# Kernel optimization log

Measured on AMD Instinct MI355X. Metric: run time of the kernel, lower is better.

The kernel has to match this reference:

```python
import jax, jax.numpy as jnp
import numpy as np
from jax import lax

SIGMA = 5
RADIUS = int(4 * SIGMA + 0.5)  # 20 -> kernel size 41, pad_size = 41//2 = 20 = RADIUS
D_AP = 2.27
D_DV = 2.27


def _gauss_d1_kernel():
    # gaussian_kernel1d(sigma, order=1, radius): q(x) = -x/sigma^2, kernel = q(x)*phi(x)
    x = np.arange(-RADIUS, RADIUS + 1).astype(np.float64)
    phi = np.exp(-0.5 / SIGMA ** 2 * x ** 2)
    phi = phi / phi.sum()
    return ((-x / SIGMA ** 2) * phi).astype(np.float32)

_KERNEL = jnp.asarray(_gauss_d1_kernel())


def _conv1d_valid(x, k):
    # x: [N, L], k: [K] -> [N, L-K+1]; cross-correlation, same as torch F.conv1d
    return lax.conv_general_dilated(x[:, None, :], k[None, None, :], (1,), 'VALID')[:, 0, :]


def diffY(x):
    # circular padding along H, derivative / dDV
    c, h, w = x.shape
    xp = jnp.pad(x, ((0, 0), (RADIUS, RADIUS), (0, 0)), mode='wrap')
    xp = jnp.transpose(xp, (0, 2, 1)).reshape(c * w, h + 2 * RADIUS)
    out = _conv1d_valid(xp, _KERNEL).reshape(c, w, h)
    return jnp.transpose(out, (0, 2, 1)) / D_DV


def diffX(x):
    # reflect padding along W, derivative / dAP
    c, h, w = x.shape
    xp = jnp.pad(x, ((0, 0), (0, 0), (RADIUS, RADIUS)), mode='reflect')
    out = _conv1d_valid(xp.reshape(c * h, w + 2 * RADIUS), _KERNEL).reshape(c, h, w)
    return out / D_AP


def setup_inputs() -> dict:
    key = jax.random.key(0)
    k1, k2, k3, k4, k5 = jax.random.split(key, 5)
    H, W = 1024, 2048
    return {
        'y': jax.random.normal(k1, (5, H, W), dtype=jnp.float32),
        'v': jax.random.normal(k2, (2, H, W), dtype=jnp.float32),
        'gamma_ds': jax.random.normal(k3, (H, W), dtype=jnp.float32),
        'cad_coefs': jax.random.uniform(k4, (3,), dtype=jnp.float32),
        'myo_coefs': jax.random.uniform(k5, (5,), dtype=jnp.float32),
    }


def reference(y, v, gamma_ds, cad_coefs, myo_coefs):
    H, W = y.shape[-2:]
    m4 = y[:4]                                  # [4,H,W] myosin components
    c1 = y[4:]                                  # [1,H,W] cadherin

    d1_m = jnp.stack([diffY(m4), diffX(m4)], axis=-1).reshape(2, 2, H, W, 2)
    m = m4.reshape(2, 2, H, W)
    d1_c = jnp.stack([diffY(c1), diffX(c1)], axis=-1).reshape(H, W, 2)
    c = c1[0]

    d1_v = jnp.stack([diffY(v), diffX(v)], axis=-1)   # [2,H,W,2]: d1_v[i,y,x,j] = d_j v_i
    gv = jnp.einsum('iyxj->ijyx', d1_v)
    gvT = jnp.einsum('jyxi->ijyx', d1_v)
    O = -0.5 * (gv - gvT)                       # vorticity
    E = 0.5 * (gv + gvT)                        # strain rate

    eye = jnp.eye(2, dtype=y.dtype)[:, :, None, None]
    trm_yx = jnp.einsum('kkyx->yx', m)
    deviatoric = m - 0.5 * trm_yx[None, None] * eye

    m_norm = jnp.sqrt(jnp.sum(m * m, axis=(0, 1), keepdims=True))            # [1,1,H,W]
    m_0 = jnp.mean(m_norm, axis=(2, 3), keepdims=True)                       # [1,1,1,1]
    dev_mag = jnp.sqrt(jnp.sum(deviatoric * deviatoric, axis=(0, 1), keepdims=True))
    devE = jnp.einsum('klyx,klyx->yx', deviatoric, E)[None, None]

    E_active = E - jnp.sign(devE) * devE * deviatoric / dev_mag ** 2
    E_active = 0.5 * E_active * dev_mag / m_0
    E_passive = E - E_active

    mE = (jnp.einsum('ikyx,kjyx->ijyx', m, E_passive)
          + jnp.einsum('ikyx,kjyx->ijyx', E_passive, m))

    cad = jax.nn.relu(cad_coefs)
    myo = jax.nn.relu(myo_coefs)

    cdot = (-jnp.einsum('iyx,yxi->yx', v, d1_c)
            - cad[0] * c
            + cad[1] * c * jnp.einsum('iyxi->yx', d1_v)
            + cad[2] * gamma_ds)

    trm = trm_yx[None, None]
    gamma_dv = jnp.array([[1.0, 0.0], [0.0, 0.0]], dtype=y.dtype)[:, :, None, None]

    mdot = (-jnp.einsum('kyx,ijyxk->ijyx', v, d1_m)
            - jnp.einsum('ikyx,kjyx->ijyx', O, m)
            + jnp.einsum('ikyx,kjyx->ijyx', m, O)
            - myo[0] * m
            + myo[1] * mE
            - myo[2] * c[None, None] * mE
            + myo[3] * trm * gamma_dv
            + myo[4] * trm * m)

    return jnp.concatenate([mdot.reshape(4, H, W), cdot[None]], axis=0)
```

## Files before the change

### kernel.cpp

```cpp
#include <hip/hip_runtime.h>
#include <math.h>

#define RAD 20
#define KLEN 41
#define NH 1024
#define NW 2048
#define NHW (NH * NW)

struct KW { float w[KLEN]; };
constexpr double cexp_neg(double u) {
  double term = 1.0, sum = 1.0;
  for (int k = 1; k < 30; ++k) { term *= (-u) / (double)k; sum += term; }
  return sum;
}
constexpr KW make_kw() {
  KW r{};
  double ph[KLEN] = {};
  double s = 0.0;
  for (int i = 0; i < KLEN; ++i) {
    double d = (double)(i - RAD);
    double e = cexp_neg(d * d / 800.0);
    e = e * e; e = e * e; e = e * e; e = e * e;
    ph[i] = e; s += e;
  }
  for (int i = 0; i < KLEN; ++i) {
    double d = (double)(i - RAD);
    r.w[i] = (float)((-d / 25.0) * (ph[i] / s) / 2.27);
  }
  return r;
}
static constexpr KW KWC = make_kw();

template <int K>
__device__ __forceinline__ void tap(float s, float& r0, float& r1, float& r2,
                                    float& r3, float& r4, float& r5, float& r6,
                                    float& r7) {
  if constexpr (K - 0 >= 0 && K - 0 <= 40) r0 = fmaf(s, KWC.w[K - 0], r0);
  if constexpr (K - 1 >= 0 && K - 1 <= 40) r1 = fmaf(s, KWC.w[K - 1], r1);
  if constexpr (K - 2 >= 0 && K - 2 <= 40) r2 = fmaf(s, KWC.w[K - 2], r2);
  if constexpr (K - 3 >= 0 && K - 3 <= 40) r3 = fmaf(s, KWC.w[K - 3], r3);
  if constexpr (K - 4 >= 0 && K - 4 <= 40) r4 = fmaf(s, KWC.w[K - 4], r4);
  if constexpr (K - 5 >= 0 && K - 5 <= 40) r5 = fmaf(s, KWC.w[K - 5], r5);
  if constexpr (K - 6 >= 0 && K - 6 <= 40) r6 = fmaf(s, KWC.w[K - 6], r6);
  if constexpr (K - 7 >= 0 && K - 7 <= 40) r7 = fmaf(s, KWC.w[K - 7], r7);
}

#define R8 r0, r1, r2, r3, r4, r5, r6, r7

__global__ __launch_bounds__(256) void k_reduce(const float* __restrict__ y,
                                                double* __restrict__ acc) {
  const int tid = blockIdx.x * blockDim.x + threadIdx.x;
  const int stride = gridDim.x * blockDim.x;
  double local = 0.0;
  for (int i = tid; i < NHW; i += stride) {
    float a = y[i];
    float b = y[i + NHW];
    float c = y[i + 2 * (size_t)NHW];
    float d = y[i + 3 * (size_t)NHW];
    local += (double)sqrtf(a * a + b * b + c * c + d * d);
  }
#pragma unroll
  for (int off = 32; off > 0; off >>= 1) local += __shfl_down(local, off, 64);
  __shared__ double smem[4];
  const int lane = threadIdx.x & 63;
  const int wid = threadIdx.x >> 6;
  if (lane == 0) smem[wid] = local;
  __syncthreads();
  if (threadIdx.x == 0) {
    double s = smem[0] + smem[1] + smem[2] + smem[3];
    atomicAdd(acc, s);
  }
}

__global__ __launch_bounds__(256) void k_dx(const float* __restrict__ y,
                                            const float* __restrict__ v,
                                            float* __restrict__ ws) {
  __shared__ float row[2120];
  const int t = threadIdx.x;
  const int r = blockIdx.x;
  const int ch = blockIdx.y;
  const float* src = (ch < 5) ? (y + (size_t)ch * NHW) : (v + (size_t)(ch - 5) * NHW);
  const float* rp = src + (size_t)r * NW;

#define SWZ(i) ((i) + ((i) >> 6))
#define ST(i, val) { const int ii_ = (i); row[SWZ(ii_)] = (val); }

  const float4* rp4 = (const float4*)rp;
  float4 b0 = rp4[t];
  float4 b1 = rp4[t + 256];
  ST(RAD + 4 * t + 0, b0.x)
  ST(RAD + 4 * t + 1, b0.y)
  ST(RAD + 4 * t + 2, b0.z)
  ST(RAD + 4 * t + 3, b0.w)
  ST(RAD + 4 * (t + 256) + 0, b1.x)
  ST(RAD + 4 * (t + 256) + 1, b1.y)
  ST(RAD + 4 * (t + 256) + 2, b1.z)
  ST(RAD + 4 * (t + 256) + 3, b1.w)
  if (t < RAD) {
    ST(t, rp[RAD - t])
    ST(NW + RAD + t, rp[NW - 2 - t])
  }
  __syncthreads();

  const int xb = 8 * t;
  float r0 = 0.f, r1 = 0.f, r2 = 0.f, r3 = 0.f;
  float r4 = 0.f, r5 = 0.f, r6 = 0.f, r7 = 0.f;
#define RD(k) { const int x_ = xb + (k); float s_ = row[SWZ(x_)]; tap<(k)>(s_, R8); }
  RD(0)  RD(1)  RD(2)  RD(3)  RD(4)  RD(5)  RD(6)  RD(7)
  RD(8)  RD(9)  RD(10) RD(11) RD(12) RD(13) RD(14) RD(15)
  RD(16) RD(17) RD(18) RD(19) RD(20) RD(21) RD(22) RD(23)
  RD(24) RD(25) RD(26) RD(27) RD(28) RD(29) RD(30) RD(31)
  RD(32) RD(33) RD(34) RD(35) RD(36) RD(37) RD(38) RD(39)
  RD(40) RD(41) RD(42) RD(43) RD(44) RD(45) RD(46) RD(47)
#undef RD

  float4 o0, o1;
  o0.x = r0; o0.y = r1; o0.z = r2; o0.w = r3;
  o1.x = r4; o1.y = r5; o1.z = r6; o1.w = r7;
  float4* dst = (float4*)(ws + (size_t)(7 + ch) * NHW + (size_t)r * NW + xb);
  dst[0] = o0;
  dst[1] = o1;
}

#define TW 64
#define TH 32

__global__ __launch_bounds__(256) void k_dy(const float* __restrict__ y,
                                            const float* __restrict__ v,
                                            float* __restrict__ ws) {
  __shared__ float tile[(TH + 2 * RAD) * TW];
  const int lane = threadIdx.x & 63;
  const int wid = threadIdx.x >> 6;
  const int x0 = blockIdx.x * TW;
  const int yb = blockIdx.y * TH;
  const int ch = blockIdx.z;
  const float* src = (ch < 5) ? (y + (size_t)ch * NHW) : (v + (size_t)(ch - 5) * NHW);

#define GLD(k) src[(size_t)(((yb - RAD + wid + 4 * (k)) + NH) & (NH - 1)) * NW + x0 + lane]
  float t0 = GLD(0), t1 = GLD(1), t2 = GLD(2), t3 = GLD(3), t4 = GLD(4);
  float t5 = GLD(5), t6 = GLD(6), t7 = GLD(7), t8 = GLD(8), t9 = GLD(9);
  float t10 = GLD(10), t11 = GLD(11), t12 = GLD(12), t13 = GLD(13);
  float t14 = GLD(14), t15 = GLD(15), t16 = GLD(16), t17 = GLD(17);
#define TST(k, val) tile[(wid + 4 * (k)) * TW + lane] = val;
  TST(0, t0)  TST(1, t1)  TST(2, t2)  TST(3, t3)  TST(4, t4)  TST(5, t5)
  TST(6, t6)  TST(7, t7)  TST(8, t8)  TST(9, t9)  TST(10, t10) TST(11, t11)
  TST(12, t12) TST(13, t13) TST(14, t14) TST(15, t15) TST(16, t16) TST(17, t17)
  __syncthreads();

  const int base = wid * 8;
  float r0 = 0.f, r1 = 0.f, r2 = 0.f, r3 = 0.f;
  float r4 = 0.f, r5 = 0.f, r6 = 0.f, r7 = 0.f;
#define DYCHUNK(c)                                                   \
  {                                                                  \
    float s0 = tile[(base + 4 * (c) + 0) * TW + lane];               \
    float s1 = tile[(base + 4 * (c) + 1) * TW + lane];               \
    float s2 = tile[(base + 4 * (c) + 2) * TW + lane];               \
    float s3 = tile[(base + 4 * (c) + 3) * TW + lane];               \
    tap<4 * (c) + 0>(s0, R8);                                        \
    tap<4 * (c) + 1>(s1, R8);                                        \
    tap<4 * (c) + 2>(s2, R8);                                        \
    tap<4 * (c) + 3>(s3, R8);                                        \
  }
  DYCHUNK(0) DYCHUNK(1) DYCHUNK(2) DYCHUNK(3) DYCHUNK(4) DYCHUNK(5)
  DYCHUNK(6) DYCHUNK(7) DYCHUNK(8) DYCHUNK(9) DYCHUNK(10) DYCHUNK(11)

  float* dst = ws + (size_t)ch * NHW + (size_t)(yb + base) * NW + x0 + lane;
  dst[0] = r0;
  dst[(size_t)NW] = r1;
  dst[2 * (size_t)NW] = r2;
  dst[3 * (size_t)NW] = r3;
  dst[4 * (size_t)NW] = r4;
  dst[5 * (size_t)NW] = r5;
  dst[6 * (size_t)NW] = r6;
  dst[7 * (size_t)NW] = r7;
}

__global__ __launch_bounds__(256) void k_final(
    const float* __restrict__ y, const float* __restrict__ v,
    const float* __restrict__ gds, const float* __restrict__ cadc,
    const float* __restrict__ myoc, const float* __restrict__ ws,
    const double* __restrict__ acc, float* __restrict__ out) {
  const size_t i = (size_t)blockIdx.x * blockDim.x + threadIdx.x;
  if (i >= NHW) return;

  const float m0 = (float)(acc[0] / (double)NHW);
  const float cad0 = fmaxf(cadc[0], 0.f);
  const float cad1 = fmaxf(cadc[1], 0.f);
  const float cad2 = fmaxf(cadc[2], 0.f);
  const float my0 = fmaxf(myoc[0], 0.f);
  const float my1 = fmaxf(myoc[1], 0.f);
  const float my2 = fmaxf(myoc[2], 0.f);
  const float my3 = fmaxf(myoc[3], 0.f);
  const float my4 = fmaxf(myoc[4], 0.f);

  const float m00 = y[i];
  const float m01 = y[i + (size_t)NHW];
  const float m10 = y[i + 2 * (size_t)NHW];
  const float m11 = y[i + 3 * (size_t)NHW];
  const float c = y[i + 4 * (size_t)NHW];
  const float v0 = v[i];
  const float v1 = v[i + (size_t)NHW];
  const float g = gds[i];

  const float dY_m00 = ws[i];
  const float dY_m01 = ws[i + (size_t)NHW];
  const float dY_m10 = ws[i + 2 * (size_t)NHW];
  const float dY_m11 = ws[i + 3 * (size_t)NHW];
  const float dY_c = ws[i + 4 * (size_t)NHW];
  const float dY_v0 = ws[i + 5 * (size_t)NHW];
  const float dY_v1 = ws[i + 6 * (size_t)NHW];
  const float dX_m00 = ws[i + 7 * (size_t)NHW];
  const float dX_m01 = ws[i + 8 * (size_t)NHW];
  const float dX_m10 = ws[i + 9 * (size_t)NHW];
  const float dX_m11 = ws[i + 10 * (size_t)NHW];
  const float dX_c = ws[i + 11 * (size_t)NHW];
  const float dX_v0 = ws[i + 12 * (size_t)NHW];
  const float dX_v1 = ws[i + 13 * (size_t)NHW];

  const float gv00 = dY_v0, gv01 = dX_v0, gv10 = dY_v1, gv11 = dX_v1;
  const float ww = -0.5f * (gv01 - gv10);
  const float E00 = gv00, E11 = gv11;
  const float E01 = 0.5f * (gv01 + gv10);
  const float E10 = E01;

  const float trm = m00 + m11;
  const float dev00 = m00 - 0.5f * trm;
  const float dev01 = m01;
  const float dev10 = m10;
  const float dev11 = m11 - 0.5f * trm;
  const float dmag_sq = dev00 * dev00 + dev01 * dev01 + dev10 * dev10 + dev11 * dev11;
  const float dm = sqrtf(dmag_sq);
  const float dm2 = dm * dm;
  const float devE = dev00 * E00 + dev01 * E01 + dev10 * E10 + dev11 * E11;
  const float sg = (devE > 0.f) ? 1.f : ((devE < 0.f) ? -1.f : 0.f);
  const float coef = sg * devE / dm2;
  const float sc = 0.5f * dm / m0;

  const float Ea00 = (E00 - coef * dev00) * sc;
  const float Ea01 = (E01 - coef * dev01) * sc;
  const float Ea10 = (E10 - coef * dev10) * sc;
  const float Ea11 = (E11 - coef * dev11) * sc;
  const float Ep00 = E00 - Ea00;
  const float Ep01 = E01 - Ea01;
  const float Ep10 = E10 - Ea10;
  const float Ep11 = E11 - Ea11;

  const float mE00 = (m00 * Ep00 + m01 * Ep10) + (Ep00 * m00 + Ep01 * m10);
  const float mE01 = (m00 * Ep01 + m01 * Ep11) + (Ep00 * m01 + Ep01 * m11);
  const float mE10 = (m10 * Ep00 + m11 * Ep10) + (Ep10 * m00 + Ep11 * m10);
  const float mE11 = (m10 * Ep01 + m11 * Ep11) + (Ep10 * m01 + Ep11 * m11);

  const float divv = gv00 + gv11;
  const float cdot = -(v0 * dY_c + v1 * dX_c) - cad0 * c + cad1 * c * divv + cad2 * g;

  const float md00 = -(v0 * dY_m00 + v1 * dX_m00) - ww * m10 - ww * m01 - my0 * m00 +
                     my1 * mE00 - my2 * c * mE00 + my3 * trm + my4 * trm * m00;
  const float md01 = -(v0 * dY_m01 + v1 * dX_m01) - ww * m11 + ww * m00 - my0 * m01 +
                     my1 * mE01 - my2 * c * mE01 + my4 * trm * m01;
  const float md10 = -(v0 * dY_m10 + v1 * dX_m10) + ww * m00 - ww * m11 - my0 * m10 +
                     my1 * mE10 - my2 * c * mE10 + my4 * trm * m10;
  const float md11 = -(v0 * dY_m11 + v1 * dX_m11) + ww * m01 + ww * m10 - my0 * m11 +
                     my1 * mE11 - my2 * c * mE11 + my4 * trm * m11;

  out[i] = md00;
  out[i + (size_t)NHW] = md01;
  out[i + 2 * (size_t)NHW] = md10;
  out[i + 3 * (size_t)NHW] = md11;
  out[i + 4 * (size_t)NHW] = cdot;
}

extern "C" void kernel_launch(void* const* d_in, const int* in_sizes, int n_in,
                              void* d_out, int out_size, void* d_ws, size_t ws_size,
                              hipStream_t stream) {
  (void)in_sizes; (void)n_in; (void)out_size; (void)ws_size;
  const float* y = (const float*)d_in[0];
  const float* v = (const float*)d_in[1];
  const float* gds = (const float*)d_in[2];
  const float* cadc = (const float*)d_in[3];
  const float* myoc = (const float*)d_in[4];
  float* out = (float*)d_out;

  double* acc = (double*)d_ws;
  float* planes = (float*)((char*)d_ws + 512);

  hipMemsetAsync(acc, 0, sizeof(double), stream);
  k_reduce<<<dim3(1024), dim3(256), 0, stream>>>(y, acc);
  k_dx<<<dim3(NH, 7), dim3(256), 0, stream>>>(y, v, planes);
  k_dy<<<dim3(NW / TW, NH / TH, 7), dim3(256), 0, stream>>>(y, v, planes);
  k_final<<<dim3(NHW / 256), dim3(256), 0, stream>>>(y, v, gds, cadc, myoc, planes, acc, out);
}
```

Before: 202.1 us.

## Fuse Y-derivative convolution into final pointwise kernel and vectorize reduction loads

Merges the vertical Gaussian-derivative stencil kernel with the final pointwise kernel. Y-derivatives for all seven channels now stay in registers instead of being written to and read back from seven workspace planes, and c, v0 and v1 are read from the shared tile. The shared tile grows to four channels (about 73 KB) and each thread holds 56 accumulators, which may reduce occupancy. The reduction kernel also switches to float4 loads.

```diff
diff --git a/kernel.cpp b/kernel.cpp
--- a/kernel.cpp
+++ b/kernel.cpp
@@ -47,17 +47,44 @@
 
 #define R8 r0, r1, r2, r3, r4, r5, r6, r7
 
+#define TW 64
+#define TH 32
+#define TILE_CH ((TH + 2 * RAD) * TW)
+
+__device__ __forceinline__ void conv_col(const float* __restrict__ t, int base,
+                                         int lane, float& r0, float& r1,
+                                         float& r2, float& r3, float& r4,
+                                         float& r5, float& r6, float& r7) {
+#define CCHUNK(c)                                      \
+  {                                                    \
+    float s0 = t[(base + 4 * (c) + 0) * TW + lane];    \
+    float s1 = t[(base + 4 * (c) + 1) * TW + lane];    \
+    float s2 = t[(base + 4 * (c) + 2) * TW + lane];    \
+    float s3 = t[(base + 4 * (c) + 3) * TW + lane];    \
+    tap<4 * (c) + 0>(s0, R8);                          \
+    tap<4 * (c) + 1>(s1, R8);                          \
+    tap<4 * (c) + 2>(s2, R8);                          \
+    tap<4 * (c) + 3>(s3, R8);                          \
+  }
+  CCHUNK(0) CCHUNK(1) CCHUNK(2) CCHUNK(3) CCHUNK(4) CCHUNK(5)
+  CCHUNK(6) CCHUNK(7) CCHUNK(8) CCHUNK(9) CCHUNK(10) CCHUNK(11)
+#undef CCHUNK
+}
+
 __global__ __launch_bounds__(256) void k_reduce(const float* __restrict__ y,
                                                 double* __restrict__ acc) {
   const int tid = blockIdx.x * blockDim.x + threadIdx.x;
   const int stride = gridDim.x * blockDim.x;
   double local = 0.0;
-  for (int i = tid; i < NHW; i += stride) {
-    float a = y[i];
-    float b = y[i + NHW];
-    float c = y[i + 2 * (size_t)NHW];
-    float d = y[i + 3 * (size_t)NHW];
-    local += (double)sqrtf(a * a + b * b + c * c + d * d);
+  for (int q = tid; q < NHW / 4; q += stride) {
+    float4 a = ((const float4*)y)[q];
+    float4 b = ((const float4*)(y + NHW))[q];
+    float4 c = ((const float4*)(y + 2 * (size_t)NHW))[q];
+    float4 d = ((const float4*)(y + 3 * (size_t)NHW))[q];
+    local += (double)sqrtf(a.x * a.x + b.x * b.x + c.x * c.x + d.x * d.x);
+    local += (double)sqrtf(a.y * a.y + b.y * b.y + c.y * c.y + d.y * d.y);
+    local += (double)sqrtf(a.z * a.z + b.z * b.z + c.z * c.z + d.z * d.z);
+    local += (double)sqrtf(a.w * a.w + b.w * b.w + c.w * c.w + d.w * d.w);
   }
 #pragma unroll
   for (int off = 32; off > 0; off >>= 1) local += __shfl_down(local, off, 64);
@@ -122,66 +149,17 @@
   dst[1] = o1;
 }
 
-#define TW 64
-#define TH 32
-
-__global__ __launch_bounds__(256) void k_dy(const float* __restrict__ y,
-                                            const float* __restrict__ v,
-                                            float* __restrict__ ws) {
-  __shared__ float tile[(TH + 2 * RAD) * TW];
+__global__ __launch_bounds__(256) void k_dyf(
+    const float* __restrict__ y, const float* __restrict__ v,
+    const float* __restrict__ gds, const float* __restrict__ cadc,
+    const float* __restrict__ myoc, const float* __restrict__ ws,
+    const double* __restrict__ acc, float* __restrict__ out) {
+  __shared__ float tile[4 * TILE_CH];
   const int lane = threadIdx.x & 63;
   const int wid = threadIdx.x >> 6;
   const int x0 = blockIdx.x * TW;
   const int yb = blockIdx.y * TH;
-  const int ch = blockIdx.z;
-  const float* src = (ch < 5) ? (y + (size_t)ch * NHW) : (v + (size_t)(ch - 5) * NHW);
-
-#define GLD(k) src[(size_t)(((yb - RAD + wid + 4 * (k)) + NH) & (NH - 1)) * NW + x0 + lane]
-  float t0 = GLD(0), t1 = GLD(1), t2 = GLD(2), t3 = GLD(3), t4 = GLD(4);
-  float t5 = GLD(5), t6 = GLD(6), t7 = GLD(7), t8 = GLD(8), t9 = GLD(9);
-  float t10 = GLD(10), t11 = GLD(11), t12 = GLD(12), t13 = GLD(13);
-  float t14 = GLD(14), t15 = GLD(15), t16 = GLD(16), t17 = GLD(17);
-#define TST(k, val) tile[(wid + 4 * (k)) * TW + lane] = val;
-  TST(0, t0)  TST(1, t1)  TST(2, t2)  TST(3, t3)  TST(4, t4)  TST(5, t5)
-  TST(6, t6)  TST(7, t7)  TST(8, t8)  TST(9, t9)  TST(10, t10) TST(11, t11)
-  TST(12, t12) TST(13, t13) TST(14, t14) TST(15, t15) TST(16, t16) TST(17, t17)
-  __syncthreads();
-
   const int base = wid * 8;
-  float r0 = 0.f, r1 = 0.f, r2 = 0.f, r3 = 0.f;
-  float r4 = 0.f, r5 = 0.f, r6 = 0.f, r7 = 0.f;
-#define DYCHUNK(c)                                                   \
-  {                                                                  \
-    float s0 = tile[(base + 4 * (c) + 0) * TW + lane];               \
-    float s1 = tile[(base + 4 * (c) + 1) * TW + lane];               \
-    float s2 = tile[(base + 4 * (c) + 2) * TW + lane];               \
-    float s3 = tile[(base + 4 * (c) + 3) * TW + lane];               \
-    tap<4 * (c) + 0>(s0, R8);                                        \
-    tap<4 * (c) + 1>(s1, R8);                                        \
-    tap<4 * (c) + 2>(s2, R8);                                        \
-    tap<4 * (c) + 3>(s3, R8);                                        \
-  }
-  DYCHUNK(0) DYCHUNK(1) DYCHUNK(2) DYCHUNK(3) DYCHUNK(4) DYCHUNK(5)
-  DYCHUNK(6) DYCHUNK(7) DYCHUNK(8) DYCHUNK(9) DYCHUNK(10) DYCHUNK(11)
-
-  float* dst = ws + (size_t)ch * NHW + (size_t)(yb + base) * NW + x0 + lane;
-  dst[0] = r0;
-  dst[(size_t)NW] = r1;
-  dst[2 * (size_t)NW] = r2;
-  dst[3 * (size_t)NW] = r3;
-  dst[4 * (size_t)NW] = r4;
-  dst[5 * (size_t)NW] = r5;
-  dst[6 * (size_t)NW] = r6;
-  dst[7 * (size_t)NW] = r7;
-}
-
-__global__ __launch_bounds__(256) void k_final(
-    const float* __restrict__ y, const float* __restrict__ v,
-    const float* __restrict__ gds, const float* __restrict__ cadc,
-    const float* __restrict__ myoc, const float* __restrict__ ws,
-    const double* __restrict__ acc, float* __restrict__ out) {
-  const size_t i = (size_t)blockIdx.x * blockDim.x + threadIdx.x;
-  if (i >= NHW) return;
 
   const float m0 = (float)(acc[0] / (double)NHW);
   const float cad0 = fmaxf(cadc[0], 0.f);
@@ -193,80 +171,134 @@
   const float my3 = fmaxf(myoc[3], 0.f);
   const float my4 = fmaxf(myoc[4], 0.f);
 
-  const float m00 = y[i];
-  const float m01 = y[i + (size_t)NHW];
-  const float m10 = y[i + 2 * (size_t)NHW];
-  const float m11 = y[i + 3 * (size_t)NHW];
-  const float c = y[i + 4 * (size_t)NHW];
-  const float v0 = v[i];
-  const float v1 = v[i + (size_t)NHW];
-  const float g = gds[i];
-
-  const float dY_m00 = ws[i];
-  const float dY_m01 = ws[i + (size_t)NHW];
-  const float dY_m10 = ws[i + 2 * (size_t)NHW];
-  const float dY_m11 = ws[i + 3 * (size_t)NHW];
-  const float dY_c = ws[i + 4 * (size_t)NHW];
-  const float dY_v0 = ws[i + 5 * (size_t)NHW];
-  const float dY_v1 = ws[i + 6 * (size_t)NHW];
-  const float dX_m00 = ws[i + 7 * (size_t)NHW];
-  const float dX_m01 = ws[i + 8 * (size_t)NHW];
-  const float dX_m10 = ws[i + 9 * (size_t)NHW];
-  const float dX_m11 = ws[i + 10 * (size_t)NHW];
-  const float dX_c = ws[i + 11 * (size_t)NHW];
-  const float dX_v0 = ws[i + 12 * (size_t)NHW];
-  const float dX_v1 = ws[i + 13 * (size_t)NHW];
-
-  const float gv00 = dY_v0, gv01 = dX_v0, gv10 = dY_v1, gv11 = dX_v1;
-  const float ww = -0.5f * (gv01 - gv10);
-  const float E00 = gv00, E11 = gv11;
-  const float E01 = 0.5f * (gv01 + gv10);
-  const float E10 = E01;
-
-  const float trm = m00 + m11;
-  const float dev00 = m00 - 0.5f * trm;
-  const float dev01 = m01;
-  const float dev10 = m10;
-  const float dev11 = m11 - 0.5f * trm;
-  const float dmag_sq = dev00 * dev00 + dev01 * dev01 + dev10 * dev10 + dev11 * dev11;
-  const float dm = sqrtf(dmag_sq);
-  const float dm2 = dm * dm;
-  const float devE = dev00 * E00 + dev01 * E01 + dev10 * E10 + dev11 * E11;
-  const float sg = (devE > 0.f) ? 1.f : ((devE < 0.f) ? -1.f : 0.f);
-  const float coef = sg * devE / dm2;
-  const float sc = 0.5f * dm / m0;
-
-  const float Ea00 = (E00 - coef * dev00) * sc;
-  const float Ea01 = (E01 - coef * dev01) * sc;
-  const float Ea10 = (E10 - coef * dev10) * sc;
-  const float Ea11 = (E11 - coef * dev11) * sc;
-  const float Ep00 = E00 - Ea00;
-  const float Ep01 = E01 - Ea01;
-  const float Ep10 = E10 - Ea10;
-  const float Ep11 = E11 - Ea11;
-
-  const float mE00 = (m00 * Ep00 + m01 * Ep10) + (Ep00 * m00 + Ep01 * m10);
-  const float mE01 = (m00 * Ep01 + m01 * Ep11) + (Ep00 * m01 + Ep01 * m11);
-  const float mE10 = (m10 * Ep00 + m11 * Ep10) + (Ep10 * m00 + Ep11 * m10);
-  const float mE11 = (m10 * Ep01 + m11 * Ep11) + (Ep10 * m01 + Ep11 * m11);
-
-  const float divv = gv00 + gv11;
-  const float cdot = -(v0 * dY_c + v1 * dX_c) - cad0 * c + cad1 * c * divv + cad2 * g;
-
-  const float md00 = -(v0 * dY_m00 + v1 * dX_m00) - ww * m10 - ww * m01 - my0 * m00 +
-                     my1 * mE00 - my2 * c * mE00 + my3 * trm + my4 * trm * m00;
-  const float md01 = -(v0 * dY_m01 + v1 * dX_m01) - ww * m11 + ww * m00 - my0 * m01 +
-                     my1 * mE01 - my2 * c * mE01 + my4 * trm * m01;
-  const float md10 = -(v0 * dY_m10 + v1 * dX_m10) + ww * m00 - ww * m11 - my0 * m10 +
-                     my1 * mE10 - my2 * c * mE10 + my4 * trm * m10;
-  const float md11 = -(v0 * dY_m11 + v1 * dX_m11) + ww * m01 + ww * m10 - my0 * m11 +
-                     my1 * mE11 - my2 * c * mE11 + my4 * trm * m11;
-
-  out[i] = md00;
-  out[i + (size_t)NHW] = md01;
-  out[i + 2 * (size_t)NHW] = md10;
-  out[i + 3 * (size_t)NHW] = md11;
-  out[i + 4 * (size_t)NHW] = cdot;
+#define SGLD(sp, k) \
+  (sp)[(size_t)(((yb - RAD + wid + 4 * (k)) + NH) & (NH - 1)) * NW + x0 + lane]
+#define STAGECH(g, srcp)                                                    \
+  {                                                                         \
+    const float* sp_ = (srcp);                                              \
+    float u0 = SGLD(sp_, 0), u1 = SGLD(sp_, 1), u2 = SGLD(sp_, 2);          \
+    float u3 = SGLD(sp_, 3), u4 = SGLD(sp_, 4), u5 = SGLD(sp_, 5);          \
+    float u6 = SGLD(sp_, 6), u7 = SGLD(sp_, 7), u8 = SGLD(sp_, 8);          \
+    float u9 = SGLD(sp_, 9), u10 = SGLD(sp_, 10), u11 = SGLD(sp_, 11);      \
+    float u12 = SGLD(sp_, 12), u13 = SGLD(sp_, 13), u14 = SGLD(sp_, 14);    \
+    float u15 = SGLD(sp_, 15), u16 = SGLD(sp_, 16), u17 = SGLD(sp_, 17);    \
+    float* tb_ = &tile[(g) * TILE_CH];                                      \
+    tb_[(wid + 0) * TW + lane] = u0;   tb_[(wid + 4) * TW + lane] = u1;     \
+    tb_[(wid + 8) * TW + lane] = u2;   tb_[(wid + 12) * TW + lane] = u3;    \
+    tb_[(wid + 16) * TW + lane] = u4;  tb_[(wid + 20) * TW + lane] = u5;    \
+    tb_[(wid + 24) * TW + lane] = u6;  tb_[(wid + 28) * TW + lane] = u7;    \
+    tb_[(wid + 32) * TW + lane] = u8;  tb_[(wid + 36) * TW + lane] = u9;    \
+    tb_[(wid + 40) * TW + lane] = u10; tb_[(wid + 44) * TW + lane] = u11;   \
+    tb_[(wid + 48) * TW + lane] = u12; tb_[(wid + 52) * TW + lane] = u13;   \
+    tb_[(wid + 56) * TW + lane] = u14; tb_[(wid + 60) * TW + lane] = u15;   \
+    tb_[(wid + 64) * TW + lane] = u16; tb_[(wid + 68) * TW + lane] = u17;   \
+  }
+
+#define DECL8(P)                                                       \
+  float P##0 = 0.f, P##1 = 0.f, P##2 = 0.f, P##3 = 0.f, P##4 = 0.f,    \
+        P##5 = 0.f, P##6 = 0.f, P##7 = 0.f;
+#define CALLCONV(g, P)                                                  \
+  conv_col(&tile[(g) * TILE_CH], base, lane, P##0, P##1, P##2, P##3,    \
+           P##4, P##5, P##6, P##7);
+
+  STAGECH(0, y)
+  STAGECH(1, y + (size_t)NHW)
+  STAGECH(2, y + 2 * (size_t)NHW)
+  STAGECH(3, y + 3 * (size_t)NHW)
+  __syncthreads();
+  DECL8(ym00) DECL8(ym01) DECL8(ym10) DECL8(ym11)
+  CALLCONV(0, ym00)
+  CALLCONV(1, ym01)
+  CALLCONV(2, ym10)
+  CALLCONV(3, ym11)
+  __syncthreads();
+
+  STAGECH(0, y + 4 * (size_t)NHW)
+  STAGECH(1, v)
+  STAGECH(2, v + (size_t)NHW)
+  __syncthreads();
+  DECL8(yc) DECL8(yv0) DECL8(yv1)
+  CALLCONV(0, yc)
+  CALLCONV(1, yv0)
+  CALLCONV(2, yv1)
+
+#define POINT(q)                                                              \
+  {                                                                           \
+    const size_t idx = (size_t)(yb + base + (q)) * NW + x0 + lane;            \
+    const int trow = (RAD + base + (q)) * TW + lane;                          \
+    const float m00 = y[idx];                                                 \
+    const float m01 = y[idx + (size_t)NHW];                                   \
+    const float m10 = y[idx + 2 * (size_t)NHW];                               \
+    const float m11 = y[idx + 3 * (size_t)NHW];                               \
+    const float c = tile[0 * TILE_CH + trow];                                 \
+    const float v0 = tile[1 * TILE_CH + trow];                                \
+    const float v1 = tile[2 * TILE_CH + trow];                                \
+    const float g = gds[idx];                                                 \
+    const float dY_m00 = ym00##q, dY_m01 = ym01##q;                           \
+    const float dY_m10 = ym10##q, dY_m11 = ym11##q;                           \
+    const float dY_c = yc##q, dY_v0 = yv0##q, dY_v1 = yv1##q;                 \
+    const float dX_m00 = ws[idx + 7 * (size_t)NHW];                           \
+    const float dX_m01 = ws[idx + 8 * (size_t)NHW];                           \
+    const float dX_m10 = ws[idx + 9 * (size_t)NHW];                           \
+    const float dX_m11 = ws[idx + 10 * (size_t)NHW];                          \
+    const float dX_c = ws[idx + 11 * (size_t)NHW];                            \
+    const float dX_v0 = ws[idx + 12 * (size_t)NHW];                           \
+    const float dX_v1 = ws[idx + 13 * (size_t)NHW];                           \
+    const float gv00 = dY_v0, gv01 = dX_v0, gv10 = dY_v1, gv11 = dX_v1;       \
+    const float ww = -0.5f * (gv01 - gv10);                                   \
+    const float E00 = gv00, E11 = gv11;                                       \
+    const float E01 = 0.5f * (gv01 + gv10);                                   \
+    const float E10 = E01;                                                    \
+    const float trm = m00 + m11;                                              \
+    const float dev00 = m00 - 0.5f * trm;                                     \
+    const float dev01 = m01;                                                  \
+    const float dev10 = m10;                                                  \
+    const float dev11 = m11 - 0.5f * trm;                                     \
+    const float dmag_sq =                                                     \
+        dev00 * dev00 + dev01 * dev01 + dev10 * dev10 + dev11 * dev11;        \
+    const float dm = sqrtf(dmag_sq);                                          \
+    const float dm2 = dm * dm;                                                \
+    const float devE = dev00 * E00 + dev01 * E01 + dev10 * E10 + dev11 * E11; \
+    const float sg = (devE > 0.f) ? 1.f : ((devE < 0.f) ? -1.f : 0.f);        \
+    const float coef = sg * devE / dm2;                                       \
+    const float sc = 0.5f * dm / m0;                                          \
+    const float Ea00 = (E00 - coef * dev00) * sc;                             \
+    const float Ea01 = (E01 - coef * dev01) * sc;                             \
+    const float Ea10 = (E10 - coef * dev10) * sc;                             \
+    const float Ea11 = (E11 - coef * dev11) * sc;                             \
+    const float Ep00 = E00 - Ea00;                                            \
+    const float Ep01 = E01 - Ea01;                                            \
+    const float Ep10 = E10 - Ea10;                                            \
+    const float Ep11 = E11 - Ea11;                                            \
+    const float mE00 = (m00 * Ep00 + m01 * Ep10) + (Ep00 * m00 + Ep01 * m10); \
+    const float mE01 = (m00 * Ep01 + m01 * Ep11) + (Ep00 * m01 + Ep01 * m11); \
+    const float mE10 = (m10 * Ep00 + m11 * Ep10) + (Ep10 * m00 + Ep11 * m10); \
+    const float mE11 = (m10 * Ep01 + m11 * Ep11) + (Ep10 * m01 + Ep11 * m11); \
+    const float divv = gv00 + gv11;                                           \
+    const float cdot =                                                        \
+        -(v0 * dY_c + v1 * dX_c) - cad0 * c + cad1 * c * divv + cad2 * g;     \
+    const float md00 = -(v0 * dY_m00 + v1 * dX_m00) - ww * m10 - ww * m01 -   \
+                       my0 * m00 + my1 * mE00 - my2 * c * mE00 + my3 * trm +  \
+                       my4 * trm * m00;                                       \
+    const float md01 = -(v0 * dY_m01 + v1 * dX_m01) - ww * m11 + ww * m00 -   \
+                       my0 * m01 + my1 * mE01 - my2 * c * mE01 +              \
+                       my4 * trm * m01;                                       \
+    const float md10 = -(v0 * dY_m10 + v1 * dX_m10) + ww * m00 - ww * m11 -   \
+                       my0 * m10 + my1 * mE10 - my2 * c * mE10 +              \
+                       my4 * trm * m10;                                       \
+    const float md11 = -(v0 * dY_m11 + v1 * dX_m11) + ww * m01 + ww * m10 -   \
+                       my0 * m11 + my1 * mE11 - my2 * c * mE11 +              \
+                       my4 * trm * m11;                                       \
+    out[idx] = md00;                                                          \
+    out[idx + (size_t)NHW] = md01;                                            \
+    out[idx + 2 * (size_t)NHW] = md10;                                        \
+    out[idx + 3 * (size_t)NHW] = md11;                                        \
+    out[idx + 4 * (size_t)NHW] = cdot;                                        \
+  }
+
+  POINT(0) POINT(1) POINT(2) POINT(3)
+  POINT(4) POINT(5) POINT(6) POINT(7)
+#undef POINT
 }
 
 extern "C" void kernel_launch(void* const* d_in, const int* in_sizes, int n_in,
@@ -286,6 +318,6 @@
   hipMemsetAsync(acc, 0, sizeof(double), stream);
   k_reduce<<<dim3(1024), dim3(256), 0, stream>>>(y, acc);
   k_dx<<<dim3(NH, 7), dim3(256), 0, stream>>>(y, v, planes);
-  k_dy<<<dim3(NW / TW, NH / TH, 7), dim3(256), 0, stream>>>(y, v, planes);
-  k_final<<<dim3(NHW / 256), dim3(256), 0, stream>>>(y, v, gds, cadc, myoc, planes, acc, out);
-}
+  k_dyf<<<dim3(NW / TW, NH / TH), dim3(256), 0, stream>>>(y, v, gds, cadc, myoc,
+                                                          planes, acc, out);
+}
```

Measured after the change: 179.7 us. -11.1%, faster.
